# Kernel tuning notes

Hardware: AMD Instinct MI355X
Metric: run time of the kernel (lower is better)

## Reference

```python
import jax, jax.numpy as jnp
import numpy as np

B, T, HID = 8, 1024, 2048
H, D = 16, 128          # num_attention_heads, head_dim (num_kv_heads = 1)
Q_RANK, KV_RANK = 128, 64
EPS = 1e-6
MIN_VAL = -1e9          # fp32 branch of create_causal_padding_mask


def _rmsnorm(x, w, eps=EPS):
    return x * jax.lax.rsqrt(jnp.mean(x * x, axis=-1, keepdims=True) + eps) * w


def _rope(x, cos, sin):
    x1, x2 = jnp.split(x, 2, axis=-1)
    return jnp.concatenate([x1 * cos - x2 * sin, x2 * cos + x1 * sin], axis=-1)


def setup_inputs() -> dict:
    key = jax.random.key(0)
    ks = jax.random.split(key, 12)
    s = lambda fan_in: 1.0 / np.sqrt(fan_in)
    return {
        'hidden_states': jax.random.normal(ks[0], (B, T, HID), jnp.float32),
        'cos_g': jax.random.uniform(ks[1], (1, T, 1, D // 2), jnp.float32, -1.0, 1.0),
        'sin_g': jax.random.uniform(ks[2], (1, T, 1, D // 2), jnp.float32, -1.0, 1.0),
        'cos_l': jax.random.uniform(ks[3], (1, T, 1, D // 2), jnp.float32, -1.0, 1.0),
        'sin_l': jax.random.uniform(ks[4], (1, T, 1, D // 2), jnp.float32, -1.0, 1.0),
        'Wq_a': jax.random.normal(ks[5], (HID, Q_RANK), jnp.float32) * s(HID),
        'bq_a': jnp.zeros((Q_RANK,), jnp.float32),
        'Wq_b': jax.random.normal(ks[6], (Q_RANK, H * D), jnp.float32) * s(Q_RANK),
        'bq_b': jnp.zeros((H * D,), jnp.float32),
        'Wkv_a': jax.random.normal(ks[7], (HID, KV_RANK), jnp.float32) * s(HID),
        'bkv_a': jnp.zeros((KV_RANK,), jnp.float32),
        'Wkv_b': jax.random.normal(ks[8], (KV_RANK, 2 * D), jnp.float32) * s(KV_RANK),
        'bkv_b': jnp.zeros((2 * D,), jnp.float32),
        'q_norm_w': jnp.ones((D,), jnp.float32),
        'kv_norm_w': jnp.ones((KV_RANK,), jnp.float32),
        'Wo': jax.random.normal(ks[9], (H * D, HID), jnp.float32) * s(H * D),
        'nope_logit': jnp.array([-2.0], jnp.float32),
        'gl_logit': jnp.array([np.log(0.01 / 0.99)], jnp.float32),
        'attention_mask': jnp.ones((B, T), jnp.int32),
    }


def reference(hidden_states, cos_g, sin_g, cos_l, sin_l,
              Wq_a, bq_a, Wq_b, bq_b, Wkv_a, bkv_a, Wkv_b, bkv_b,
              q_norm_w, kv_norm_w, Wo, nope_logit, gl_logit, attention_mask):
    h = hidden_states
    # learned global/local RoPE blend
    a = jax.nn.sigmoid(gl_logit).reshape(1, 1, 1, 1)
    cos = cos_g * a + cos_l * (1.0 - a)
    sin = sin_g * a + sin_l * (1.0 - a)

    # LoRA q path: q_b(RMSNorm(q_a(h)))
    q = _rmsnorm(h @ Wq_a + bq_a, q_norm_w) @ Wq_b + bq_b      # [B,T,H*D]
    q = q.reshape(B, T, H, D)
    q_pe = _rope(q, cos, sin)

    # LoRA kv path: kv_b(RMSNorm(kv_a(h)))  (single kv head)
    kv = _rmsnorm(h @ Wkv_a + bkv_a, kv_norm_w) @ Wkv_b + bkv_b  # [B,T,2*D]
    k, v = jnp.split(kv, 2, axis=-1)                            # [B,T,D] each
    k_pe = _rope(k.reshape(B, T, 1, D), cos, sin)[:, :, 0, :]   # [B,T,D]

    # nope/rope alpha mix
    na = jax.nn.sigmoid(nope_logit).reshape(1, 1, 1, 1)
    q_f = na * q + (1.0 - na) * q_pe                            # [B,T,H,D]
    k_f = na[..., 0] * k + (1.0 - na[..., 0]) * k_pe            # [B,T,D]

    # causal + padding additive mask
    causal = jnp.triu(jnp.ones((T, T), bool), k=1)              # [T,T]
    pad = (attention_mask == 0)[:, None, None, :]               # [B,1,1,T]
    add_mask = jnp.where(causal[None, None] | pad, MIN_VAL, 0.0).astype(h.dtype)

    scale = D ** -0.5
    scores = jnp.einsum('bthd,bsd->bhts', q_f, k_f) * scale + add_mask
    attn = jax.nn.softmax(scores, axis=-1)                      # [B,H,T,T]
    out = jnp.einsum('bhts,bsd->bthd', attn, v)                 # [B,T,H,D]
    return out.reshape(B, T, H * D) @ Wo
```

## Files before the change

kernel.cpp:

```cpp
#include <hip/hip_runtime.h>
#include <hip/hip_bf16.h>

typedef __attribute__((ext_vector_type(8))) short bf16x8;
typedef __attribute__((ext_vector_type(4))) float f32x4;
typedef __attribute__((ext_vector_type(4))) unsigned short us4;

#define DEV __device__ __forceinline__

constexpr int Bc = 8, Tc = 1024, HIDc = 2048, Hc = 16, Dc = 128;
constexpr int ROWSc = Bc * Tc;

DEV unsigned short f2bfb(float x) {
  union { float f; unsigned u; } v; v.f = x;
  unsigned r = v.u + 0x7fffu + ((v.u >> 16) & 1u);
  return (unsigned short)(r >> 16);
}
DEV float bfb2f(unsigned short b) {
  union { unsigned u; float f; } v; v.u = ((unsigned)b) << 16; return v.f;
}
DEV float fexp2(float x) { return __builtin_amdgcn_exp2f(x); }
DEV unsigned pkbf(float lo, float hi) {
  union { float f; unsigned u; } a, b; a.f = lo; b.f = hi;
  return ((b.u + 0x8000u) & 0xffff0000u) | ((a.u + 0x8000u) >> 16);
}

DEV void gload16(const void* g, void* l) {
  __builtin_amdgcn_global_load_lds(
      (const __attribute__((address_space(1))) unsigned int*)g,
      (__attribute__((address_space(3))) unsigned int*)l, 16, 0, 0);
}


__global__ void k_blend(const float* __restrict__ cg, const float* __restrict__ sg,
                        const float* __restrict__ cl, const float* __restrict__ sl,
                        const float* __restrict__ gl,
                        float* __restrict__ cosb, float* __restrict__ sinb) {
  int u = blockIdx.x * 256 + threadIdx.x;
  if (u >= Tc * 64) return;
  float a = 1.0f / (1.0f + __expf(-gl[0]));
  cosb[u] = cg[u] * a + cl[u] * (1.0f - a);
  sinb[u] = sg[u] * a + sl[u] * (1.0f - a);
}

__global__ void k_zero(unsigned short* __restrict__ p, int n) {
  int i = blockIdx.x * 256 + threadIdx.x;
  if (i < n) p[i] = 0;
}

__global__ __launch_bounds__(256) void k_transpose(const float* __restrict__ in,
                                                   unsigned short* __restrict__ out,
                                                   int R, int C) {
  __shared__ float tile[32][33];
  int tx = threadIdx.x & 31, ty = threadIdx.x >> 5;
  int r0 = blockIdx.y * 32, c0 = blockIdx.x * 32;
#pragma unroll
  for (int i = 0; i < 4; i++)
    tile[ty + i * 8][tx] = in[(size_t)(r0 + ty + i * 8) * C + c0 + tx];
  __syncthreads();
#pragma unroll
  for (int i = 0; i < 4; i++) {
    int rr = ty + i * 8;
    out[(size_t)(c0 + rr) * R + r0 + tx] = f2bfb(tile[tx][rr]);
  }
}


__global__ __launch_bounds__(256) void k_gemm1(const float* __restrict__ A,
                                               const unsigned short* __restrict__ Bt,
                                               float* __restrict__ C0,
                                               float* __restrict__ C1) {
  constexpr int K = 2048, N = 256, KH = 1024, NT = KH / 32;
  __shared__ __align__(16) unsigned short Als[2][64 * 32];
  __shared__ __align__(16) unsigned short Bls[2][128 * 32];
  int lin = blockIdx.x;
  int wg = (lin & 7) * 64 + (lin >> 3);
  int ksl = wg & 1;
  int nti = (wg >> 1) & 1;
  int mti = wg >> 2;
  int m0 = mti * 64, n0 = nti * 128, k0 = ksl * KH;
  float* C = ksl ? C1 : C0;
  int tid = threadIdx.x, lane = tid & 63, wc = tid >> 6;
  int ar = tid >> 2, akc = (tid & 3) * 8;
  const float* Ag = A + (size_t)(m0 + ar) * K + k0 + akc;
  const unsigned short* Bg0 = Bt + (size_t)(n0 + ar) * K + k0 + akc;
  const unsigned short* Bg1 = Bt + (size_t)(n0 + 64 + ar) * K + k0 + akc;
  f32x4 acc[4][2];
  f32x4 zz = {0.f, 0.f, 0.f, 0.f};
#pragma unroll
  for (int m = 0; m < 4; m++)
#pragma unroll
    for (int n = 0; n < 2; n++) acc[m][n] = zz;
  int fr = lane & 15, fk = (lane >> 4) * 8;

  float4 a0 = *(const float4*)(Ag);
  float4 a1 = *(const float4*)(Ag + 4);
  gload16(Bg0, &Bls[0][tid * 8]);
  gload16(Bg1, &Bls[0][2048 + tid * 8]);
  {
    us4 c0v = { f2bfb(a0.x), f2bfb(a0.y), f2bfb(a0.z), f2bfb(a0.w) };
    us4 c1v = { f2bfb(a1.x), f2bfb(a1.y), f2bfb(a1.z), f2bfb(a1.w) };
    *(us4*)&Als[0][ar * 32 + akc] = c0v;
    *(us4*)&Als[0][ar * 32 + akc + 4] = c1v;
  }
  a0 = *(const float4*)(Ag + 32);
  a1 = *(const float4*)(Ag + 36);
  __syncthreads();

  for (int t = 0; t < NT; t++) {
    int cur = t & 1, nxt = cur ^ 1;
    if (t + 1 < NT) {
      gload16(Bg0 + (t + 1) * 32, &Bls[nxt][tid * 8]);
      gload16(Bg1 + (t + 1) * 32, &Bls[nxt][2048 + tid * 8]);
    }
    bf16x8 af[4], bfv[2];
#pragma unroll
    for (int i = 0; i < 4; i++)
      af[i] = *(const bf16x8*)&Als[cur][(i * 16 + fr) * 32 + fk];
#pragma unroll
    for (int i = 0; i < 2; i++)
      bfv[i] = *(const bf16x8*)&Bls[cur][(wc * 32 + i * 16 + fr) * 32 + fk];
    __builtin_amdgcn_s_setprio(1);
#pragma unroll
    for (int m = 0; m < 4; m++)
#pragma unroll
      for (int n = 0; n < 2; n++)
        acc[m][n] = __builtin_amdgcn_mfma_f32_16x16x32_bf16(af[m], bfv[n], acc[m][n], 0, 0, 0);
    __builtin_amdgcn_s_setprio(0);
    if (t + 1 < NT) {
      us4 d0 = { f2bfb(a0.x), f2bfb(a0.y), f2bfb(a0.z), f2bfb(a0.w) };
      us4 d1 = { f2bfb(a1.x), f2bfb(a1.y), f2bfb(a1.z), f2bfb(a1.w) };
      *(us4*)&Als[nxt][ar * 32 + akc] = d0;
      *(us4*)&Als[nxt][ar * 32 + akc + 4] = d1;
    }
    if (t + 2 < NT) {
      a0 = *(const float4*)(Ag + (t + 2) * 32);
      a1 = *(const float4*)(Ag + (t + 2) * 32 + 4);
    }
    __syncthreads();
  }
  int gg = lane >> 4;
#pragma unroll
  for (int m = 0; m < 4; m++)
#pragma unroll
    for (int n = 0; n < 2; n++)
#pragma unroll
      for (int r = 0; r < 4; r++) {
        size_t row = (size_t)m0 + m * 16 + gg * 4 + r;
        size_t col = (size_t)n0 + wc * 32 + n * 16 + fr;
        C[row * N + col] = acc[m][n][r];
      }
}


template <int OUTB>
__global__ __launch_bounds__(256) void k_gemm(const unsigned short* __restrict__ A,
                                              const unsigned short* __restrict__ Bt,
                                              void* __restrict__ outp,
                                              int M, int N, int K, int nx) {
  __shared__ __align__(16) unsigned short As[4096];
  __shared__ __align__(16) unsigned short Bs[4096];
  int lin = blockIdx.x;
  int qq = gridDim.x >> 3;
  int wg = (lin & 7) * qq + (lin >> 3);
  int m0 = (wg / nx) * 128, n0 = (wg % nx) * 128;
  int tid = threadIdx.x;
  int lane = tid & 63;
  int wave = tid >> 6;
  int wr = wave >> 1, wc = wave & 1;
  int srow = tid >> 2;
  int skc = (tid & 3) * 8;
  const unsigned short* Ag0 = A + (size_t)(m0 + srow) * K + skc;
  const unsigned short* Ag1 = A + (size_t)(m0 + 64 + srow) * K + skc;
  const unsigned short* Bg0 = Bt + (size_t)(n0 + srow) * K + skc;
  const unsigned short* Bg1 = Bt + (size_t)(n0 + 64 + srow) * K + skc;
  unsigned short* Asl0 = &As[tid * 8];
  unsigned short* Asl1 = &As[2048 + tid * 8];
  unsigned short* Bsl0 = &Bs[tid * 8];
  unsigned short* Bsl1 = &Bs[2048 + tid * 8];
  f32x4 acc[4][4];
  f32x4 zz = {0.f, 0.f, 0.f, 0.f};
#pragma unroll
  for (int m = 0; m < 4; m++)
#pragma unroll
    for (int n = 0; n < 4; n++) acc[m][n] = zz;
  int fr = lane & 15, fk = (lane >> 4) * 8;
  for (int kt = 0; kt < K; kt += 32) {
    __syncthreads();
    gload16(Ag0 + kt, Asl0);
    gload16(Ag1 + kt, Asl1);
    gload16(Bg0 + kt, Bsl0);
    gload16(Bg1 + kt, Bsl1);
    __syncthreads();
    bf16x8 af[4], bfv[4];
#pragma unroll
    for (int i = 0; i < 4; i++)
      af[i] = *(const bf16x8*)&As[(wr * 64 + i * 16 + fr) * 32 + fk];
#pragma unroll
    for (int i = 0; i < 4; i++)
      bfv[i] = *(const bf16x8*)&Bs[(wc * 64 + i * 16 + fr) * 32 + fk];
    __builtin_amdgcn_s_setprio(1);
#pragma unroll
    for (int m = 0; m < 4; m++)
#pragma unroll
      for (int n = 0; n < 4; n++)
        acc[m][n] = __builtin_amdgcn_mfma_f32_16x16x32_bf16(af[m], bfv[n], acc[m][n], 0, 0, 0);
    __builtin_amdgcn_s_setprio(0);
  }
  int gg = lane >> 4;
#pragma unroll
  for (int m = 0; m < 4; m++)
#pragma unroll
    for (int n = 0; n < 4; n++)
#pragma unroll
      for (int r = 0; r < 4; r++) {
        size_t row = (size_t)m0 + wr * 64 + m * 16 + gg * 4 + r;
        size_t col = (size_t)n0 + wc * 64 + n * 16 + fr;
        if (OUTB)
          ((unsigned short*)outp)[row * N + col] = f2bfb(acc[m][n][r]);
        else
          ((float*)outp)[row * N + col] = acc[m][n][r];
      }
}


__global__ __launch_bounds__(512, 2) void k_gemm3(const unsigned short* __restrict__ A,
                                                  const unsigned short* __restrict__ Bt,
                                                  float* __restrict__ C) {
  constexpr int K = 2048, N = 2048, NT = K / 64;
  __shared__ __align__(16) unsigned short Als[2][2][8192];
  __shared__ __align__(16) unsigned short Bls[2][2][8192];
  int lin = blockIdx.x;
  int wg = (lin & 7) * 32 + (lin >> 3);
  int m0 = (wg >> 3) * 256, n0 = (wg & 7) * 256;
  int tid = threadIdx.x, lane = tid & 63, wave = tid >> 6;
  int wm = wave >> 2, wn = wave & 3;
  int g = lane >> 4, c = lane & 15;

  int rb = tid >> 2;
  int sch = (tid & 3) ^ ((tid >> 3) & 3);
  const unsigned short* Ag = A + (size_t)(m0 + rb) * K + sch * 8;
  const unsigned short* Bg = Bt + (size_t)(n0 + rb) * K + sch * 8;
  const int gsw = (g ^ ((c >> 1) & 3)) * 8;

  f32x4 acc[8][4];
  f32x4 zz = {0.f, 0.f, 0.f, 0.f};
#pragma unroll
  for (int mi = 0; mi < 8; mi++)
#pragma unroll
    for (int ni = 0; ni < 4; ni++) acc[mi][ni] = zz;

#pragma unroll
  for (int sl = 0; sl < 2; sl++) {
    gload16(Ag + sl * 32, &Als[0][sl][tid * 8]);
    gload16(Ag + (size_t)128 * K + sl * 32, &Als[0][sl][4096 + tid * 8]);
    gload16(Bg + sl * 32, &Bls[0][sl][tid * 8]);
    gload16(Bg + (size_t)128 * K + sl * 32, &Bls[0][sl][4096 + tid * 8]);
  }

  for (int t = 0; t < NT; ++t) {
    int buf = t & 1, nb = buf ^ 1;
    bool nl = (t + 1 < NT);
    int nkt = (t + 1) * 64;
#pragma unroll
    for (int sl = 0; sl < 2; sl++) {
      if (sl == 0 || nl) {
        asm volatile("s_waitcnt vmcnt(4)" ::: "memory");
      } else {
        asm volatile("s_waitcnt vmcnt(0)" ::: "memory");
      }
      __builtin_amdgcn_sched_barrier(0);
      __builtin_amdgcn_s_barrier();
      __builtin_amdgcn_sched_barrier(0);
      const unsigned short* As_ = &Als[buf][sl][0];
      const unsigned short* Bs_ = &Bls[buf][sl][0];
      bf16x8 af[8], bfv[4];
#pragma unroll
      for (int mi = 0; mi < 8; mi++)
        af[mi] = *(const bf16x8*)&As_[(wm * 128 + mi * 16 + c) * 32 + gsw];
#pragma unroll
      for (int ni = 0; ni < 4; ni++)
        bfv[ni] = *(const bf16x8*)&Bs_[(wn * 64 + ni * 16 + c) * 32 + gsw];
      if (nl) {
        gload16(Ag + nkt + sl * 32, &Als[nb][sl][tid * 8]);
        gload16(Ag + (size_t)128 * K + nkt + sl * 32, &Als[nb][sl][4096 + tid * 8]);
      }
      __builtin_amdgcn_s_setprio(1);
#pragma unroll
      for (int mi = 0; mi < 8; mi++) {
        acc[mi][0] = __builtin_amdgcn_mfma_f32_16x16x32_bf16(af[mi], bfv[0], acc[mi][0], 0, 0, 0);
        acc[mi][1] = __builtin_amdgcn_mfma_f32_16x16x32_bf16(af[mi], bfv[1], acc[mi][1], 0, 0, 0);
      }
      __builtin_amdgcn_s_setprio(0);
      if (nl) {
        gload16(Bg + nkt + sl * 32, &Bls[nb][sl][tid * 8]);
        gload16(Bg + (size_t)128 * K + nkt + sl * 32, &Bls[nb][sl][4096 + tid * 8]);
      }
      __builtin_amdgcn_s_setprio(1);
#pragma unroll
      for (int mi = 0; mi < 8; mi++) {
        acc[mi][2] = __builtin_amdgcn_mfma_f32_16x16x32_bf16(af[mi], bfv[2], acc[mi][2], 0, 0, 0);
        acc[mi][3] = __builtin_amdgcn_mfma_f32_16x16x32_bf16(af[mi], bfv[3], acc[mi][3], 0, 0, 0);
      }
      __builtin_amdgcn_s_setprio(0);
    }
  }

#pragma unroll
  for (int mi = 0; mi < 8; mi++)
#pragma unroll
    for (int ni = 0; ni < 4; ni++)
#pragma unroll
      for (int r = 0; r < 4; r++) {
        size_t row = (size_t)m0 + wm * 128 + mi * 16 + g * 4 + r;
        size_t col = (size_t)n0 + wn * 64 + ni * 16 + c;
        C[row * N + col] = acc[mi][ni][r];
      }
}


__global__ __launch_bounds__(256) void k_gemm2q(const unsigned short* __restrict__ A,
                                                const unsigned short* __restrict__ Bt,
                                                const float* __restrict__ bqb,
                                                const float* __restrict__ cosb,
                                                const float* __restrict__ sinb,
                                                const float* __restrict__ nl,
                                                unsigned short* __restrict__ Qf) {
  constexpr int K = 128, N = 2048;
  __shared__ __align__(16) unsigned short As[4096];
  __shared__ __align__(16) unsigned short Bs[4096];
  __shared__ __align__(16) unsigned short Qt[128 * 128];
  int lin = blockIdx.x;
  int wg = (lin & 7) * 128 + (lin >> 3);
  int m0 = (wg >> 4) * 128, n0 = (wg & 15) * 128;
  int h = n0 >> 7;
  int b = m0 >> 10, t0 = m0 & 1023;
  int tid = threadIdx.x;
  int lane = tid & 63;
  int wave = tid >> 6;
  int wr = wave >> 1, wc = wave & 1;
  int srow = tid >> 2;
  int skc = (tid & 3) * 8;
  const unsigned short* Ag0 = A + (size_t)(m0 + srow) * K + skc;
  const unsigned short* Ag1 = A + (size_t)(m0 + 64 + srow) * K + skc;
  const unsigned short* Bg0 = Bt + (size_t)(n0 + srow) * K + skc;
  const unsigned short* Bg1 = Bt + (size_t)(n0 + 64 + srow) * K + skc;
  unsigned short* Asl0 = &As[tid * 8];
  unsigned short* Asl1 = &As[2048 + tid * 8];
  unsigned short* Bsl0 = &Bs[tid * 8];
  unsigned short* Bsl1 = &Bs[2048 + tid * 8];
  f32x4 acc[4][4];
  f32x4 zz = {0.f, 0.f, 0.f, 0.f};
#pragma unroll
  for (int m = 0; m < 4; m++)
#pragma unroll
    for (int n = 0; n < 4; n++) acc[m][n] = zz;
  int fr = lane & 15, fk = (lane >> 4) * 8;
  for (int kt = 0; kt < K; kt += 32) {
    __syncthreads();
    gload16(Ag0 + kt, Asl0);
    gload16(Ag1 + kt, Asl1);
    gload16(Bg0 + kt, Bsl0);
    gload16(Bg1 + kt, Bsl1);
    __syncthreads();
    bf16x8 af[4], bfv[4];
#pragma unroll
    for (int i = 0; i < 4; i++)
      af[i] = *(const bf16x8*)&As[(wr * 64 + i * 16 + fr) * 32 + fk];
#pragma unroll
    for (int i = 0; i < 4; i++)
      bfv[i] = *(const bf16x8*)&Bs[(wc * 64 + i * 16 + fr) * 32 + fk];
    __builtin_amdgcn_s_setprio(1);
#pragma unroll
    for (int m = 0; m < 4; m++)
#pragma unroll
      for (int n = 0; n < 4; n++)
        acc[m][n] = __builtin_amdgcn_mfma_f32_16x16x32_bf16(af[m], bfv[n], acc[m][n], 0, 0, 0);
    __builtin_amdgcn_s_setprio(0);
  }
  int gg = lane >> 4;
#pragma unroll
  for (int n = 0; n < 4; n++) {
    int col = wc * 64 + n * 16 + fr;
    float bias = bqb[h * 128 + col];
    int ch = col >> 3, wi = col & 7;
#pragma unroll
    for (int m = 0; m < 4; m++)
#pragma unroll
      for (int r = 0; r < 4; r++) {
        int lrow = wr * 64 + m * 16 + gg * 4 + r;
        Qt[lrow * 128 + ((ch ^ (lrow & 7)) << 3) + wi] = f2bfb(acc[m][n][r] + bias);
      }
  }
  __syncthreads();
  const float SCLQ = 0.08838834764831845f * 1.4426950408889634f;
  float na = 1.0f / (1.0f + __expf(-nl[0]));
  float nb = 1.0f - na;
#pragma unroll
  for (int it = 0; it < 4; it++) {
    int task = it * 256 + tid;
    int lrow = task >> 3, cp = task & 7;
    int t = t0 + lrow;
    bf16x8 v1 = *(const bf16x8*)&Qt[lrow * 128 + ((cp ^ (lrow & 7)) << 3)];
    bf16x8 v2 = *(const bf16x8*)&Qt[lrow * 128 + (((cp + 8) ^ (lrow & 7)) << 3)];
    float4 cA = *(const float4*)(cosb + t * 64 + cp * 8);
    float4 cB = *(const float4*)(cosb + t * 64 + cp * 8 + 4);
    float4 sA = *(const float4*)(sinb + t * 64 + cp * 8);
    float4 sB = *(const float4*)(sinb + t * 64 + cp * 8 + 4);
    float cv[8] = {cA.x, cA.y, cA.z, cA.w, cB.x, cB.y, cB.z, cB.w};
    float sv[8] = {sA.x, sA.y, sA.z, sA.w, sB.x, sB.y, sB.z, sB.w};
    float f1[8], f2[8];
#pragma unroll
    for (int j = 0; j < 8; j++) {
      float q1 = bfb2f((unsigned short)v1[j]);
      float q2 = bfb2f((unsigned short)v2[j]);
      float p1 = q1 * cv[j] - q2 * sv[j];
      float p2 = q2 * cv[j] + q1 * sv[j];
      f1[j] = (na * q1 + nb * p1) * SCLQ;
      f2[j] = (na * q2 + nb * p2) * SCLQ;
    }
    unsigned short* ob = Qf + ((size_t)(b * Hc + h) * Tc + t) * Dc + cp * 8;
    us4 o0 = {f2bfb(f1[0]), f2bfb(f1[1]), f2bfb(f1[2]), f2bfb(f1[3])};
    us4 o1 = {f2bfb(f1[4]), f2bfb(f1[5]), f2bfb(f1[6]), f2bfb(f1[7])};
    us4 o2 = {f2bfb(f2[0]), f2bfb(f2[1]), f2bfb(f2[2]), f2bfb(f2[3])};
    us4 o3 = {f2bfb(f2[4]), f2bfb(f2[5]), f2bfb(f2[6]), f2bfb(f2[7])};
    *(us4*)(ob) = o0;
    *(us4*)(ob + 4) = o1;
    *(us4*)(ob + 64) = o2;
    *(us4*)(ob + 68) = o3;
  }
}


__global__ __launch_bounds__(256) void k_norm(const float* __restrict__ A1,
                                              const float* __restrict__ A1b,
                                              const float* __restrict__ bqa,
                                              const float* __restrict__ bkva,
                                              const float* __restrict__ qw,
                                              const float* __restrict__ kvw,
                                              unsigned short* __restrict__ Qn,
                                              unsigned short* __restrict__ Kvn) {
  int wave = threadIdx.x >> 6, lane = threadIdx.x & 63;
  int row = blockIdx.x * 4 + wave;
  const float* a = A1 + (size_t)row * 256;
  const float* a2 = A1b + (size_t)row * 256;
  float x0 = a[lane] + a2[lane] + bqa[lane];
  float x1 = a[64 + lane] + a2[64 + lane] + bqa[64 + lane];
  float ss = x0 * x0 + x1 * x1;
#pragma unroll
  for (int off = 1; off < 64; off <<= 1) ss += __shfl_xor(ss, off);
  float sc = rsqrtf(ss * (1.0f / 128.0f) + 1e-6f);
  Qn[(size_t)row * 128 + lane] = f2bfb(x0 * sc * qw[lane]);
  Qn[(size_t)row * 128 + 64 + lane] = f2bfb(x1 * sc * qw[64 + lane]);
  float y = a[128 + lane] + a2[128 + lane] + bkva[lane];
  float s2 = y * y;
#pragma unroll
  for (int off = 1; off < 64; off <<= 1) s2 += __shfl_xor(s2, off);
  float sc2 = rsqrtf(s2 * (1.0f / 64.0f) + 1e-6f);
  Kvn[(size_t)row * 64 + lane] = f2bfb(y * sc2 * kvw[lane]);
}


__global__ __launch_bounds__(256) void k_rope_kv(const unsigned short* __restrict__ kvr,
                                                 const float* __restrict__ bkvb,
                                                 const float* __restrict__ cosb,
                                                 const float* __restrict__ sinb,
                                                 const float* __restrict__ nl,
                                                 unsigned short* __restrict__ Kf,
                                                 unsigned short* __restrict__ Vt) {
  int u = blockIdx.x * 256 + threadIdx.x;
  int row = u >> 6, d = u & 63;
  int t = row & (Tc - 1), b = row >> 10;
  float na = 1.0f / (1.0f + __expf(-nl[0]));
  const unsigned short* kp = kvr + (size_t)row * 256;
  float k1 = bfb2f(kp[d]) + bkvb[d];
  float k2 = bfb2f(kp[64 + d]) + bkvb[64 + d];
  float v1 = bfb2f(kp[128 + d]) + bkvb[128 + d];
  float v2 = bfb2f(kp[192 + d]) + bkvb[192 + d];
  float cv = cosb[t * 64 + d], sv = sinb[t * 64 + d];
  float p1 = k1 * cv - k2 * sv;
  float p2 = k2 * cv + k1 * sv;
  float f1 = na * k1 + (1.0f - na) * p1;
  float f2 = na * k2 + (1.0f - na) * p2;
  unsigned short* kb = Kf + (size_t)row * Dc;
  kb[d] = f2bfb(f1);
  kb[64 + d] = f2bfb(f2);
  Vt[((size_t)b * Dc + d) * Tc + t] = f2bfb(v1);
  Vt[((size_t)b * Dc + 64 + d) * Tc + t] = f2bfb(v2);
}


__global__ __launch_bounds__(512, 1) void k_attn(const unsigned short* __restrict__ Qf,
                                                 const unsigned short* __restrict__ Kf,
                                                 const unsigned short* __restrict__ Vt,
                                                 const int* __restrict__ amask,
                                                 unsigned short* __restrict__ O) {
  __shared__ __align__(16) unsigned short Ks[2][64 * 128];
  __shared__ __align__(16) unsigned short Vs[2][128 * 64];
  __shared__ __align__(16) unsigned short Plds[8][32 * 64];
  __shared__ int s_anyzero;

  int bid = blockIdx.x;
  int b = bid & 7;
  int pr = (bid >> 3) & 1;
  int h = bid >> 4;
  int tid = threadIdx.x;
  int wave = tid >> 6, lane = tid & 63;
  int g = lane >> 4, c = lane & 15;

  const unsigned short* Kp = Kf + (size_t)b * Tc * Dc;
  const unsigned short* Vp = Vt + (size_t)b * Dc * Tc;
  const int* mp = amask + b * Tc;
  char* PwB = (char*)&Plds[wave][0];
  f32x4 zz = {0.f, 0.f, 0.f, 0.f};

  if (tid == 0) s_anyzero = 0;
  __syncthreads();
  if (mp[tid] == 0 || mp[tid + 512] == 0) s_anyzero = 1;
  __syncthreads();
  bool anyz = (s_anyzero != 0);

  int kr_ = tid >> 3, kc_ = tid & 7;
  int vr_ = tid >> 2, vc_ = tid & 3;
  int kidx0 = kr_ * 128 + ((kc_ ^ (kr_ & 7)) << 3);
  int kidx1 = kr_ * 128 + (((kc_ + 8) ^ (kr_ & 7)) << 3);
  int vidx0 = vr_ * 64 + ((vc_ ^ (vr_ & 7)) << 3);
  int vidx1 = vr_ * 64 + (((vc_ + 4) ^ (vr_ & 7)) << 3);

  int c7s = (c & 7) << 4;
  int g4 = g * 4;

  for (int pass = 0; pass < 2; pass++) {
    int sp = (pass == 0) ? pr : 3 - pr;
    int qw0 = sp * 256 + wave * 32;
    int nt = (sp + 1) * 4;
    const unsigned short* Qp = Qf + ((size_t)(b * Hc + h) * Tc + qw0) * Dc;
    bf16x8 qfr[2][4];
#pragma unroll
    for (int m = 0; m < 2; m++)
#pragma unroll
      for (int ks = 0; ks < 4; ks++)
        qfr[m][ks] = *(const bf16x8*)(Qp + (size_t)(m * 16 + c) * Dc + ks * 32 + g * 8);

    f32x4 Oacc[2][8];
#pragma unroll
    for (int m = 0; m < 2; m++)
#pragma unroll
      for (int i = 0; i < 8; i++) Oacc[m][i] = zz;
    float m_r[2] = {-1e30f, -1e30f};
    float l_r[2] = {0.f, 0.f};

    bf16x8 krg[2], vrg[2];
    krg[0] = *(const bf16x8*)(Kp + (size_t)kr_ * Dc + kc_ * 8);
    krg[1] = *(const bf16x8*)(Kp + (size_t)kr_ * Dc + kc_ * 8 + 64);
    vrg[0] = *(const bf16x8*)(Vp + (size_t)vr_ * Tc + vc_ * 8);
    vrg[1] = *(const bf16x8*)(Vp + (size_t)vr_ * Tc + vc_ * 8 + 32);
    __syncthreads();
    *(bf16x8*)&Ks[0][kidx0] = krg[0];
    *(bf16x8*)&Ks[0][kidx1] = krg[1];
    *(bf16x8*)&Vs[0][vidx0] = vrg[0];
    *(bf16x8*)&Vs[0][vidx1] = vrg[1];
    __syncthreads();

    for (int st = 0; st < nt; st++) {
      int cur = st & 1;
      int s0 = st << 6;
      if (st + 1 < nt) {
        int s1 = s0 + 64;
        krg[0] = *(const bf16x8*)(Kp + (size_t)(s1 + kr_) * Dc + kc_ * 8);
        krg[1] = *(const bf16x8*)(Kp + (size_t)(s1 + kr_) * Dc + kc_ * 8 + 64);
        vrg[0] = *(const bf16x8*)(Vp + (size_t)vr_ * Tc + s1 + vc_ * 8);
        vrg[1] = *(const bf16x8*)(Vp + (size_t)vr_ * Tc + s1 + vc_ * 8 + 32);
      }

      if (s0 <= qw0 + 31) {
        const unsigned short* Kc = &Ks[cur][0];
        const unsigned short* Vc = &Vs[cur][0];

        f32x4 S[2][4];
#pragma unroll
        for (int m = 0; m < 2; m++)
#pragma unroll
          for (int j = 0; j < 4; j++) S[m][j] = zz;
        __builtin_amdgcn_s_setprio(1);
#pragma unroll
        for (int ks = 0; ks < 4; ks++)
#pragma unroll
          for (int j = 0; j < 4; j++) {
            bf16x8 kfr = *(const bf16x8*)&Kc[(j * 16 + c) * 128 + (((ks * 4 + g) ^ (c & 7)) << 3)];
            S[0][j] = __builtin_amdgcn_mfma_f32_16x16x32_bf16(kfr, qfr[0][ks], S[0][j], 0, 0, 0);
            S[1][j] = __builtin_amdgcn_mfma_f32_16x16x32_bf16(kfr, qfr[1][ks], S[1][j], 0, 0, 0);
          }
        __builtin_amdgcn_s_setprio(0);

        if (anyz) {
#pragma unroll
          for (int j = 0; j < 4; j++)
#pragma unroll
            for (int r = 0; r < 4; r++) {
              float madd = (mp[s0 + j * 16 + g4 + r] == 0) ? -2e9f : 0.0f;
              S[0][j][r] += madd;
              S[1][j][r] += madd;
            }
        }
        if (s0 + 63 > qw0) {
#pragma unroll
          for (int j = 0; j < 4; j++) {
            int kk = s0 + j * 16 + g4;
#pragma unroll
            for (int r = 0; r < 4; r++) {
#pragma unroll
              for (int m = 0; m < 2; m++)
                if (kk + r > qw0 + m * 16 + c) S[m][j][r] = -1e30f;
            }
          }
        }

        float tmax[2];
#pragma unroll
        for (int m = 0; m < 2; m++) {
          float t0 = fmaxf(fmaxf(S[m][0][0], S[m][0][1]), fmaxf(S[m][0][2], S[m][0][3]));
          float t1 = fmaxf(fmaxf(S[m][1][0], S[m][1][1]), fmaxf(S[m][1][2], S[m][1][3]));
          float t2 = fmaxf(fmaxf(S[m][2][0], S[m][2][1]), fmaxf(S[m][2][2], S[m][2][3]));
          float t3 = fmaxf(fmaxf(S[m][3][0], S[m][3][1]), fmaxf(S[m][3][2], S[m][3][3]));
          float t = fmaxf(fmaxf(t0, t1), fmaxf(t2, t3));
          t = fmaxf(t, __shfl_xor(t, 16));
          t = fmaxf(t, __shfl_xor(t, 32));
          tmax[m] = t;
        }
        bool upd = (tmax[0] > m_r[0] + 11.0f) || (tmax[1] > m_r[1] + 11.0f);
        if (__any(upd)) {
#pragma unroll
          for (int m = 0; m < 2; m++) {
            float mn = fmaxf(m_r[m], tmax[m]);
            float al = fexp2(m_r[m] - mn);
            m_r[m] = mn;
            l_r[m] *= al;
#pragma unroll
            for (int r = 0; r < 4; r++) {
              float alr = __shfl(al, (lane & 48) | (g4 + r));
#pragma unroll
              for (int j2 = 0; j2 < 8; j2++) Oacc[m][j2][r] *= alr;
            }
          }
        }

#pragma unroll
        for (int m = 0; m < 2; m++) {
          int rowb = (m * 16 + c) * 128;
#pragma unroll
          for (int j = 0; j < 4; j++) {
            float e0 = fexp2(S[m][j][0] - m_r[m]);
            float e1 = fexp2(S[m][j][1] - m_r[m]);
            float e2 = fexp2(S[m][j][2] - m_r[m]);
            float e3 = fexp2(S[m][j][3] - m_r[m]);
            l_r[m] += (e0 + e1) + (e2 + e3);
            uint2 w;
            w.x = pkbf(e0, e1);
            w.y = pkbf(e2, e3);
            int inrow = (j * 32 + g * 8) ^ c7s;
            *(uint2*)(PwB + rowb + inrow) = w;
          }
        }

        asm volatile("s_waitcnt lgkmcnt(0)" ::: "memory");
        bf16x8 pa[2][2];
#pragma unroll
        for (int m = 0; m < 2; m++)
#pragma unroll
          for (int sk = 0; sk < 2; sk++)
            pa[m][sk] = *(const bf16x8*)(PwB + (m * 16 + c) * 128 + (((sk * 64 + g * 16)) ^ c7s));
        __builtin_amdgcn_s_setprio(1);
#pragma unroll
        for (int sk = 0; sk < 2; sk++)
#pragma unroll
          for (int j2 = 0; j2 < 8; j2++) {
            int row = j2 * 16 + c;
            bf16x8 vfr = *(const bf16x8*)&Vc[row * 64 + (((sk * 4 + g) ^ (row & 7)) << 3)];
            Oacc[0][j2] = __builtin_amdgcn_mfma_f32_16x16x32_bf16(pa[0][sk], vfr, Oacc[0][j2], 0, 0, 0);
            Oacc[1][j2] = __builtin_amdgcn_mfma_f32_16x16x32_bf16(pa[1][sk], vfr, Oacc[1][j2], 0, 0, 0);
          }
        __builtin_amdgcn_s_setprio(0);
      }

      if (st + 1 < nt) {
        int nxt = cur ^ 1;
        *(bf16x8*)&Ks[nxt][kidx0] = krg[0];
        *(bf16x8*)&Ks[nxt][kidx1] = krg[1];
        *(bf16x8*)&Vs[nxt][vidx0] = vrg[0];
        *(bf16x8*)&Vs[nxt][vidx1] = vrg[1];
      }
      __syncthreads();
    }

#pragma unroll
    for (int m = 0; m < 2; m++) {
      float lt = l_r[m];
      lt += __shfl_xor(lt, 16);
      lt += __shfl_xor(lt, 32);
      float inv = 1.0f / lt;
#pragma unroll
      for (int r = 0; r < 4; r++) {
        float invr = __shfl(inv, (lane & 48) | (g4 + r));
        int qr = qw0 + m * 16 + g4 + r;
        unsigned short* ob = O + ((size_t)(b * Tc) + qr) * HIDc + h * Dc;
#pragma unroll
        for (int j2 = 0; j2 < 8; j2++) ob[j2 * 16 + c] = f2bfb(Oacc[m][j2][r] * invr);
      }
    }
  }
}


extern "C" void kernel_launch(void* const* d_in, const int* in_sizes, int n_in,
                              void* d_out, int out_size, void* d_ws, size_t ws_size,
                              hipStream_t stream) {
  const float* h = (const float*)d_in[0];
  const float* cg = (const float*)d_in[1];
  const float* sg = (const float*)d_in[2];
  const float* cl = (const float*)d_in[3];
  const float* sl = (const float*)d_in[4];
  const float* Wq_a = (const float*)d_in[5];
  const float* bq_a = (const float*)d_in[6];
  const float* Wq_b = (const float*)d_in[7];
  const float* bq_b = (const float*)d_in[8];
  const float* Wkv_a = (const float*)d_in[9];
  const float* bkv_a = (const float*)d_in[10];
  const float* Wkv_b = (const float*)d_in[11];
  const float* bkv_b = (const float*)d_in[12];
  const float* qw = (const float*)d_in[13];
  const float* kvw = (const float*)d_in[14];
  const float* Wo = (const float*)d_in[15];
  const float* nl = (const float*)d_in[16];
  const float* gl = (const float*)d_in[17];
  const int* am = (const int*)d_in[18];
  float* out = (float*)d_out;
  char* ws = (char*)d_ws;

  const size_t o_hB = 0;
  const size_t o_A1b = 33554432;
  const size_t o_Qf = 67108864;
  const size_t o_A1 = 100663296;
  const size_t o_Qn = 109051904;
  const size_t o_Kvn = 111149056;
  const size_t o_kvr = 112197632;
  const size_t o_Kf = 116391936;
  const size_t o_Vt = 118489088;
  const size_t o_W1t = 120586240;
  const size_t o_Wqbt = 121634816;
  const size_t o_Wkbt = 122159104;
  const size_t o_Wot = 122191872;
  const size_t o_cos = 130580480;
  const size_t o_sin = 130842624;

  unsigned short* Obuf = (unsigned short*)(ws + o_hB);
  float* A1b = (float*)(ws + o_A1b);
  unsigned short* Qf = (unsigned short*)(ws + o_Qf);
  float* A1 = (float*)(ws + o_A1);
  unsigned short* Qn = (unsigned short*)(ws + o_Qn);
  unsigned short* Kvn = (unsigned short*)(ws + o_Kvn);
  unsigned short* kvr = (unsigned short*)(ws + o_kvr);
  unsigned short* Kf = (unsigned short*)(ws + o_Kf);
  unsigned short* Vt = (unsigned short*)(ws + o_Vt);
  unsigned short* W1t = (unsigned short*)(ws + o_W1t);
  unsigned short* Wqbt = (unsigned short*)(ws + o_Wqbt);
  unsigned short* Wkbt = (unsigned short*)(ws + o_Wkbt);
  unsigned short* Wot = (unsigned short*)(ws + o_Wot);
  float* cosb = (float*)(ws + o_cos);
  float* sinb = (float*)(ws + o_sin);

  (void)in_sizes; (void)n_in; (void)out_size; (void)ws_size;

  k_blend<<<256, 256, 0, stream>>>(cg, sg, cl, sl, gl, cosb, sinb);
  k_zero<<<512, 256, 0, stream>>>(W1t + (size_t)192 * 2048, 64 * 2048);
  k_transpose<<<dim3(4, 64), 256, 0, stream>>>(Wq_a, W1t, 2048, 128);
  k_transpose<<<dim3(2, 64), 256, 0, stream>>>(Wkv_a, W1t + (size_t)128 * 2048, 2048, 64);
  k_transpose<<<dim3(64, 4), 256, 0, stream>>>(Wq_b, Wqbt, 128, 2048);
  k_transpose<<<dim3(8, 2), 256, 0, stream>>>(Wkv_b, Wkbt, 64, 256);
  k_transpose<<<dim3(64, 64), 256, 0, stream>>>(Wo, Wot, 2048, 2048);

  k_gemm1<<<512, 256, 0, stream>>>(h, W1t, A1, A1b);
  k_norm<<<2048, 256, 0, stream>>>(A1, A1b, bq_a, bkv_a, qw, kvw, Qn, Kvn);
  k_gemm2q<<<1024, 256, 0, stream>>>(Qn, Wqbt, bq_b, cosb, sinb, nl, Qf);
  k_gemm<1><<<128, 256, 0, stream>>>(Kvn, Wkbt, kvr, ROWSc, 256, 64, 2);
  k_rope_kv<<<2048, 256, 0, stream>>>(kvr, bkv_b, cosb, sinb, nl, Kf, Vt);
  k_attn<<<256, 512, 0, stream>>>(Qf, Kf, Vt, am, Obuf);
  k_gemm3<<<256, 512, 0, stream>>>(Obuf, Wot, out);
}
```

Measured before the change: 216.3 us.

## Fuse KV up-projection with RoPE epilogue and double-buffer gemm2q loads

Replaces the generic KV gemm plus separate k_rope_kv kernel with a single kernel. It computes the 64-row by 256-column KV tile in LDS using swizzled layouts, then applies bias, RoPE and the nope mix, and writes K plus a coalesced transposed V. This drops the kvr round trip and one launch. Separately, gemm2q now double-buffers its LDS tiles so the next K-slice loads while the current one computes. The cost is more LDS per block and fewer blocks (128) for the KV kernel.

```diff
diff --git a/kernel.cpp b/kernel.cpp
--- a/kernel.cpp
+++ b/kernel.cpp
@@ -152,77 +152,6 @@
 }
 
 
-template <int OUTB>
-__global__ __launch_bounds__(256) void k_gemm(const unsigned short* __restrict__ A,
-                                              const unsigned short* __restrict__ Bt,
-                                              void* __restrict__ outp,
-                                              int M, int N, int K, int nx) {
-  __shared__ __align__(16) unsigned short As[4096];
-  __shared__ __align__(16) unsigned short Bs[4096];
-  int lin = blockIdx.x;
-  int qq = gridDim.x >> 3;
-  int wg = (lin & 7) * qq + (lin >> 3);
-  int m0 = (wg / nx) * 128, n0 = (wg % nx) * 128;
-  int tid = threadIdx.x;
-  int lane = tid & 63;
-  int wave = tid >> 6;
-  int wr = wave >> 1, wc = wave & 1;
-  int srow = tid >> 2;
-  int skc = (tid & 3) * 8;
-  const unsigned short* Ag0 = A + (size_t)(m0 + srow) * K + skc;
-  const unsigned short* Ag1 = A + (size_t)(m0 + 64 + srow) * K + skc;
-  const unsigned short* Bg0 = Bt + (size_t)(n0 + srow) * K + skc;
-  const unsigned short* Bg1 = Bt + (size_t)(n0 + 64 + srow) * K + skc;
-  unsigned short* Asl0 = &As[tid * 8];
-  unsigned short* Asl1 = &As[2048 + tid * 8];
-  unsigned short* Bsl0 = &Bs[tid * 8];
-  unsigned short* Bsl1 = &Bs[2048 + tid * 8];
-  f32x4 acc[4][4];
-  f32x4 zz = {0.f, 0.f, 0.f, 0.f};
-#pragma unroll
-  for (int m = 0; m < 4; m++)
-#pragma unroll
-    for (int n = 0; n < 4; n++) acc[m][n] = zz;
-  int fr = lane & 15, fk = (lane >> 4) * 8;
-  for (int kt = 0; kt < K; kt += 32) {
-    __syncthreads();
-    gload16(Ag0 + kt, Asl0);
-    gload16(Ag1 + kt, Asl1);
-    gload16(Bg0 + kt, Bsl0);
-    gload16(Bg1 + kt, Bsl1);
-    __syncthreads();
-    bf16x8 af[4], bfv[4];
-#pragma unroll
-    for (int i = 0; i < 4; i++)
-      af[i] = *(const bf16x8*)&As[(wr * 64 + i * 16 + fr) * 32 + fk];
-#pragma unroll
-    for (int i = 0; i < 4; i++)
-      bfv[i] = *(const bf16x8*)&Bs[(wc * 64 + i * 16 + fr) * 32 + fk];
-    __builtin_amdgcn_s_setprio(1);
-#pragma unroll
-    for (int m = 0; m < 4; m++)
-#pragma unroll
-      for (int n = 0; n < 4; n++)
-        acc[m][n] = __builtin_amdgcn_mfma_f32_16x16x32_bf16(af[m], bfv[n], acc[m][n], 0, 0, 0);
-    __builtin_amdgcn_s_setprio(0);
-  }
-  int gg = lane >> 4;
-#pragma unroll
-  for (int m = 0; m < 4; m++)
-#pragma unroll
-    for (int n = 0; n < 4; n++)
-#pragma unroll
-      for (int r = 0; r < 4; r++) {
-        size_t row = (size_t)m0 + wr * 64 + m * 16 + gg * 4 + r;
-        size_t col = (size_t)n0 + wc * 64 + n * 16 + fr;
-        if (OUTB)
-          ((unsigned short*)outp)[row * N + col] = f2bfb(acc[m][n][r]);
-        else
-          ((float*)outp)[row * N + col] = acc[m][n][r];
-      }
-}
-
-
 __global__ __launch_bounds__(512, 2) void k_gemm3(const unsigned short* __restrict__ A,
                                                   const unsigned short* __restrict__ Bt,
                                                   float* __restrict__ C) {
@@ -325,9 +254,9 @@
                                                 const float* __restrict__ sinb,
                                                 const float* __restrict__ nl,
                                                 unsigned short* __restrict__ Qf) {
-  constexpr int K = 128, N = 2048;
-  __shared__ __align__(16) unsigned short As[4096];
-  __shared__ __align__(16) unsigned short Bs[4096];
+  constexpr int K = 128, N = 2048, NT = 4;
+  __shared__ __align__(16) unsigned short As[2][4096];
+  __shared__ __align__(16) unsigned short Bs[2][4096];
   __shared__ __align__(16) unsigned short Qt[128 * 128];
   int lin = blockIdx.x;
   int wg = (lin & 7) * 128 + (lin >> 3);
@@ -344,10 +273,6 @@
   const unsigned short* Ag1 = A + (size_t)(m0 + 64 + srow) * K + skc;
   const unsigned short* Bg0 = Bt + (size_t)(n0 + srow) * K + skc;
   const unsigned short* Bg1 = Bt + (size_t)(n0 + 64 + srow) * K + skc;
-  unsigned short* Asl0 = &As[tid * 8];
-  unsigned short* Asl1 = &As[2048 + tid * 8];
-  unsigned short* Bsl0 = &Bs[tid * 8];
-  unsigned short* Bsl1 = &Bs[2048 + tid * 8];
   f32x4 acc[4][4];
   f32x4 zz = {0.f, 0.f, 0.f, 0.f};
 #pragma unroll
@@ -355,20 +280,29 @@
 #pragma unroll
     for (int n = 0; n < 4; n++) acc[m][n] = zz;
   int fr = lane & 15, fk = (lane >> 4) * 8;
-  for (int kt = 0; kt < K; kt += 32) {
-    __syncthreads();
-    gload16(Ag0 + kt, Asl0);
-    gload16(Ag1 + kt, Asl1);
-    gload16(Bg0 + kt, Bsl0);
-    gload16(Bg1 + kt, Bsl1);
-    __syncthreads();
+
+  gload16(Ag0, &As[0][tid * 8]);
+  gload16(Ag1, &As[0][2048 + tid * 8]);
+  gload16(Bg0, &Bs[0][tid * 8]);
+  gload16(Bg1, &Bs[0][2048 + tid * 8]);
+  __syncthreads();
+
+  for (int t = 0; t < NT; t++) {
+    int cur = t & 1, nxt = cur ^ 1;
+    if (t + 1 < NT) {
+      int kt = (t + 1) * 32;
+      gload16(Ag0 + kt, &As[nxt][tid * 8]);
+      gload16(Ag1 + kt, &As[nxt][2048 + tid * 8]);
+      gload16(Bg0 + kt, &Bs[nxt][tid * 8]);
+      gload16(Bg1 + kt, &Bs[nxt][2048 + tid * 8]);
+    }
     bf16x8 af[4], bfv[4];
 #pragma unroll
     for (int i = 0; i < 4; i++)
-      af[i] = *(const bf16x8*)&As[(wr * 64 + i * 16 + fr) * 32 + fk];
+      af[i] = *(const bf16x8*)&As[cur][(wr * 64 + i * 16 + fr) * 32 + fk];
 #pragma unroll
     for (int i = 0; i < 4; i++)
-      bfv[i] = *(const bf16x8*)&Bs[(wc * 64 + i * 16 + fr) * 32 + fk];
+      bfv[i] = *(const bf16x8*)&Bs[cur][(wc * 64 + i * 16 + fr) * 32 + fk];
     __builtin_amdgcn_s_setprio(1);
 #pragma unroll
     for (int m = 0; m < 4; m++)
@@ -376,6 +310,7 @@
       for (int n = 0; n < 4; n++)
         acc[m][n] = __builtin_amdgcn_mfma_f32_16x16x32_bf16(af[m], bfv[n], acc[m][n], 0, 0, 0);
     __builtin_amdgcn_s_setprio(0);
+    __syncthreads();
   }
   int gg = lane >> 4;
 #pragma unroll
@@ -427,6 +362,104 @@
     *(us4*)(ob + 4) = o1;
     *(us4*)(ob + 64) = o2;
     *(us4*)(ob + 68) = o3;
+  }
+}
+
+
+__global__ __launch_bounds__(256) void k_gemm2kv(const unsigned short* __restrict__ A,
+                                                 const unsigned short* __restrict__ Bt,
+                                                 const float* __restrict__ bkvb,
+                                                 const float* __restrict__ cosb,
+                                                 const float* __restrict__ sinb,
+                                                 const float* __restrict__ nl,
+                                                 unsigned short* __restrict__ Kf,
+                                                 unsigned short* __restrict__ Vt) {
+  __shared__ __align__(16) unsigned short As2[64 * 64];
+  __shared__ __align__(16) unsigned short Bs2[256 * 64];
+  __shared__ __align__(16) unsigned short KVt[64 * 256];
+  int m0 = blockIdx.x * 64;
+  int b = m0 >> 10, t0 = m0 & 1023;
+  int tid = threadIdx.x, lane = tid & 63, wc = tid >> 6;
+  int fr = lane & 15, gg = lane >> 4;
+#pragma unroll
+  for (int p = 0; p < 2; p++) {
+    int slot = p * 256 + tid;
+    int row = slot >> 3, chpos = slot & 7;
+    gload16(A + (size_t)(m0 + row) * 64 + ((chpos ^ (row & 7)) << 3),
+            &As2[slot * 8]);
+  }
+#pragma unroll
+  for (int p = 0; p < 8; p++) {
+    int slot = p * 256 + tid;
+    int row = slot >> 3, chpos = slot & 7;
+    gload16(Bt + (size_t)row * 64 + ((chpos ^ (row & 7)) << 3),
+            &Bs2[slot * 8]);
+  }
+  __syncthreads();
+  f32x4 acc[4][4];
+  f32x4 zz = {0.f, 0.f, 0.f, 0.f};
+#pragma unroll
+  for (int m = 0; m < 4; m++)
+#pragma unroll
+    for (int n = 0; n < 4; n++) acc[m][n] = zz;
+#pragma unroll
+  for (int ks = 0; ks < 2; ks++) {
+    bf16x8 af[4], bfv[4];
+#pragma unroll
+    for (int m = 0; m < 4; m++) {
+      int row = m * 16 + fr;
+      af[m] = *(const bf16x8*)&As2[row * 64 + (((ks * 4 + gg) ^ (row & 7)) << 3)];
+    }
+#pragma unroll
+    for (int n = 0; n < 4; n++) {
+      int row = wc * 64 + n * 16 + fr;
+      bfv[n] = *(const bf16x8*)&Bs2[row * 64 + (((ks * 4 + gg) ^ (row & 7)) << 3)];
+    }
+#pragma unroll
+    for (int m = 0; m < 4; m++)
+#pragma unroll
+      for (int n = 0; n < 4; n++)
+        acc[m][n] = __builtin_amdgcn_mfma_f32_16x16x32_bf16(af[m], bfv[n], acc[m][n], 0, 0, 0);
+  }
+#pragma unroll
+  for (int n = 0; n < 4; n++) {
+    int col = wc * 64 + n * 16 + fr;
+    float bias = bkvb[col];
+#pragma unroll
+    for (int m = 0; m < 4; m++)
+#pragma unroll
+      for (int r = 0; r < 4; r++) {
+        int lrow = m * 16 + gg * 4 + r;
+        KVt[lrow * 256 + col] = f2bfb(acc[m][n][r] + bias);
+      }
+  }
+  __syncthreads();
+  float na = 1.0f / (1.0f + __expf(-nl[0]));
+  float nb = 1.0f - na;
+#pragma unroll
+  for (int it = 0; it < 16; it++) {
+    int idx = it * 256 + tid;
+    int row = idx >> 6, d = idx & 63;
+    int t = t0 + row;
+    float k1 = bfb2f(KVt[row * 256 + d]);
+    float k2 = bfb2f(KVt[row * 256 + 64 + d]);
+    float cv = cosb[t * 64 + d], sv = sinb[t * 64 + d];
+    float p1 = k1 * cv - k2 * sv;
+    float p2 = k2 * cv + k1 * sv;
+    unsigned short* kb = Kf + ((size_t)(b * Tc) + t) * Dc;
+    kb[d] = f2bfb(na * k1 + nb * p1);
+    kb[64 + d] = f2bfb(na * k2 + nb * p2);
+  }
+  {
+    int d = tid & 127, half = tid >> 7;
+    unsigned short* vb = Vt + ((size_t)(b * Dc) + d) * Tc + t0 + half * 32;
+#pragma unroll
+    for (int j = 0; j < 8; j++) {
+      int tl = half * 32 + j * 4;
+      us4 o = { KVt[(tl + 0) * 256 + 128 + d], KVt[(tl + 1) * 256 + 128 + d],
+                KVt[(tl + 2) * 256 + 128 + d], KVt[(tl + 3) * 256 + 128 + d] };
+      *(us4*)(vb + j * 4) = o;
+    }
   }
 }
 
@@ -457,35 +490,6 @@
   for (int off = 1; off < 64; off <<= 1) s2 += __shfl_xor(s2, off);
   float sc2 = rsqrtf(s2 * (1.0f / 64.0f) + 1e-6f);
   Kvn[(size_t)row * 64 + lane] = f2bfb(y * sc2 * kvw[lane]);
-}
-
-
-__global__ __launch_bounds__(256) void k_rope_kv(const unsigned short* __restrict__ kvr,
-                                                 const float* __restrict__ bkvb,
-                                                 const float* __restrict__ cosb,
-                                                 const float* __restrict__ sinb,
-                                                 const float* __restrict__ nl,
-                                                 unsigned short* __restrict__ Kf,
-                                                 unsigned short* __restrict__ Vt) {
-  int u = blockIdx.x * 256 + threadIdx.x;
-  int row = u >> 6, d = u & 63;
-  int t = row & (Tc - 1), b = row >> 10;
-  float na = 1.0f / (1.0f + __expf(-nl[0]));
-  const unsigned short* kp = kvr + (size_t)row * 256;
-  float k1 = bfb2f(kp[d]) + bkvb[d];
-  float k2 = bfb2f(kp[64 + d]) + bkvb[64 + d];
-  float v1 = bfb2f(kp[128 + d]) + bkvb[128 + d];
-  float v2 = bfb2f(kp[192 + d]) + bkvb[192 + d];
-  float cv = cosb[t * 64 + d], sv = sinb[t * 64 + d];
-  float p1 = k1 * cv - k2 * sv;
-  float p2 = k2 * cv + k1 * sv;
-  float f1 = na * k1 + (1.0f - na) * p1;
-  float f2 = na * k2 + (1.0f - na) * p2;
-  unsigned short* kb = Kf + (size_t)row * Dc;
-  kb[d] = f2bfb(f1);
-  kb[64 + d] = f2bfb(f2);
-  Vt[((size_t)b * Dc + d) * Tc + t] = f2bfb(v1);
-  Vt[((size_t)b * Dc + 64 + d) * Tc + t] = f2bfb(v2);
 }
 
 
@@ -742,7 +746,6 @@
   const size_t o_A1 = 100663296;
   const size_t o_Qn = 109051904;
   const size_t o_Kvn = 111149056;
-  const size_t o_kvr = 112197632;
   const size_t o_Kf = 116391936;
   const size_t o_Vt = 118489088;
   const size_t o_W1t = 120586240;
@@ -758,7 +761,6 @@
   float* A1 = (float*)(ws + o_A1);
   unsigned short* Qn = (unsigned short*)(ws + o_Qn);
   unsigned short* Kvn = (unsigned short*)(ws + o_Kvn);
-  unsigned short* kvr = (unsigned short*)(ws + o_kvr);
   unsigned short* Kf = (unsigned short*)(ws + o_Kf);
   unsigned short* Vt = (unsigned short*)(ws + o_Vt);
   unsigned short* W1t = (unsigned short*)(ws + o_W1t);
@@ -781,8 +783,7 @@
   k_gemm1<<<512, 256, 0, stream>>>(h, W1t, A1, A1b);
   k_norm<<<2048, 256, 0, stream>>>(A1, A1b, bq_a, bkv_a, qw, kvw, Qn, Kvn);
   k_gemm2q<<<1024, 256, 0, stream>>>(Qn, Wqbt, bq_b, cosb, sinb, nl, Qf);
-  k_gemm<1><<<128, 256, 0, stream>>>(Kvn, Wkbt, kvr, ROWSc, 256, 64, 2);
-  k_rope_kv<<<2048, 256, 0, stream>>>(kvr, bkv_b, cosb, sinb, nl, Kf, Vt);
+  k_gemm2kv<<<128, 256, 0, stream>>>(Kvn, Wkbt, bkv_b, cosb, sinb, nl, Kf, Vt);
   k_attn<<<256, 512, 0, stream>>>(Qf, Kf, Vt, am, Obuf);
   k_gemm3<<<256, 512, 0, stream>>>(Obuf, Wot, out);
 }
```

Measured after the change: 206.2 us. 1.05x faster.
